# Kernel tuning notes

Hardware: AMD Instinct MI355X
Metric: run time of the kernel (lower is better)

## Reference

```python
import jax, jax.numpy as jnp
import numpy as np

N = 2_097_152  # total atoms
G = 32_768     # number of graphs (~64 atoms each)
EPS = 1e-4     # sign-detection threshold from the original code


def setup_inputs() -> dict:
    key = jax.random.key(0)
    k1, k2 = jax.random.split(key)
    pos = jax.random.normal(k1, (N, 3), dtype=jnp.float32) * 3.0
    batch = jnp.sort(jax.random.randint(k2, (N,), 0, G))
    return {"pos": pos, "batch": batch, "num_graphs": G}


def reference(pos, batch, num_graphs):
    n = pos.shape[0]
    dtype = pos.dtype

    # per-graph centroid (scatter_mean)
    counts = jax.ops.segment_sum(jnp.ones((n,), dtype), batch, num_segments=num_graphs)
    center = jax.ops.segment_sum(pos, batch, num_segments=num_graphs) / jnp.maximum(counts, 1.0)[:, None]
    pc = pos - center[batch]                      # [N,3] centered positions

    # per-atom inertia contribution: r^2 * I - p p^T, then scatter_add per graph
    r_sq = jnp.sum(pc * pc, axis=-1)              # [N]
    outer = jnp.einsum('ni,nj->nij', pc, pc)      # [N,3,3]
    I_atom = r_sq[:, None, None] * jnp.eye(3, dtype=dtype) - outer
    I_mol = jax.ops.segment_sum(I_atom, batch, num_segments=num_graphs)  # [G,3,3]

    L, Q = jnp.linalg.eigh(I_mol)                 # Q: [G,3,3], columns = principal axes

    # projections of centered positions onto the (pre-flip) eigenbasis.
    # NOTE: in the torch loop, p_proj is computed once before any sign flips, and
    # flipping column 0 does not affect p_proj[:,1], so axes 0 and 1 are independent.
    proj = jnp.einsum('ni,nij->nj', pc, Q[batch])  # [N,3]

    idx = jnp.arange(n)

    def axis_sign(a):
        # parallel "first atom (in original order) with |proj| > EPS" per graph
        qual = jnp.abs(proj[:, a]) > EPS
        key_idx = jnp.where(qual, idx, n)
        first = jax.ops.segment_min(key_idx, batch, num_segments=num_graphs)  # [G]
        found = first < n
        val = proj[jnp.minimum(first, n - 1), a]
        return jnp.where(found & (val < 0), -1.0, 1.0).astype(dtype)

    s0 = axis_sign(0)
    s1 = axis_sign(1)
    q0 = Q[:, :, 0] * s0[:, None]
    q1 = Q[:, :, 1] * s1[:, None]
    q2 = jnp.cross(q0, q1)  # enforce right-handed frame
    return jnp.stack([q0, q1, q2], axis=-1)       # [G,3,3]
```

## Files before the change

kernel.cpp:

```cpp
#include <hip/hip_runtime.h>
#include <math.h>

#define CANON_EPS 1e-4f

__global__ __launch_bounds__(256) void build_starts_kernel(
    const int* __restrict__ batch, int* __restrict__ wsi, int n, int G) {
  int t = (int)(blockIdx.x * (unsigned)blockDim.x + threadIdx.x);
  int base = t * 4;
  if (base >= n) return;

  int b0, b1, b2, b3;
  if (base + 4 <= n) {
    int4 b4 = *reinterpret_cast<const int4*>(batch + base);
    b0 = b4.x; b1 = b4.y; b2 = b4.z; b3 = b4.w;
  } else {
    b0 = batch[base];
    b1 = (base + 1 < n) ? batch[base + 1] : b0;
    b2 = (base + 2 < n) ? batch[base + 2] : b1;
    b3 = (base + 3 < n) ? batch[base + 3] : b2;
  }
  int bp = (base > 0) ? batch[base - 1] : -1;

  int B[4] = {b0, b1, b2, b3};
#pragma unroll
  for (int j = 0; j < 4; ++j) {
    int i = base + j;
    if (i >= n) break;
    int prev = (j == 0) ? bp : B[j - 1];
    int b = B[j];
    for (int g = prev + 1; g <= b; ++g) wsi[g] = i;
    if (i == n - 1) {
      for (int g = b + 1; g <= G; ++g) wsi[g] = n;
    }
  }
}

__global__ __launch_bounds__(256) void moments_kernel(
    const float* __restrict__ pos, const int* __restrict__ wsi,
    float* __restrict__ wsf, int G) {
  int tid = (int)(blockIdx.x * (unsigned)blockDim.x + threadIdx.x);
  int gid = tid >> 4;
  int sub = tid & 15;
  if (gid >= G) return;

  int s = wsi[gid];
  int e = wsi[gid + 1];
  int cnt = e - s;

  float sx = 0.f, sy = 0.f, sz = 0.f;
  float sxx = 0.f, syy = 0.f, szz = 0.f, sxy = 0.f, sxz = 0.f, syz = 0.f;

#pragma unroll
  for (int k = 0; k < 5; ++k) {
    int i = s + sub + 16 * k;
    bool in = i < e;
    int ii = in ? i : 0;
    float m = in ? 1.0f : 0.0f;
    float x = pos[3 * ii + 0] * m;
    float y = pos[3 * ii + 1] * m;
    float z = pos[3 * ii + 2] * m;
    sx += x; sy += y; sz += z;
    sxx = fmaf(x, x, sxx); syy = fmaf(y, y, syy); szz = fmaf(z, z, szz);
    sxy = fmaf(x, y, sxy); sxz = fmaf(x, z, sxz); syz = fmaf(y, z, syz);
  }
  for (int i = s + 80 + sub; i < e; i += 16) {
    float x = pos[3 * i + 0];
    float y = pos[3 * i + 1];
    float z = pos[3 * i + 2];
    sx += x; sy += y; sz += z;
    sxx = fmaf(x, x, sxx); syy = fmaf(y, y, szz * 0.f + syy); szz = fmaf(z, z, szz);
    sxy = fmaf(x, y, sxy); sxz = fmaf(x, z, sxz); syz = fmaf(y, z, syz);
  }

#define RED16(v)                                                             \
  v += __shfl_xor(v, 1); v += __shfl_xor(v, 2);                              \
  v += __shfl_xor(v, 4); v += __shfl_xor(v, 8);
  RED16(sx) RED16(sy) RED16(sz)
  RED16(sxx) RED16(syy) RED16(szz)
  RED16(sxy) RED16(sxz) RED16(syz)
#undef RED16

  float fn = (float)(cnt > 0 ? cnt : 1);
  float inv = 1.0f / fn;
  float mx = sx * inv, my = sy * inv, mz = sz * inv;
  float Sxx = fmaf(-fn * mx, mx, sxx);
  float Syy = fmaf(-fn * my, my, syy);
  float Szz = fmaf(-fn * mz, mz, szz);
  float Sxy = fmaf(-fn * mx, my, sxy);
  float Sxz = fmaf(-fn * mx, mz, sxz);
  float Syz = fmaf(-fn * my, mz, syz);

  float v = mx;
  v = (sub == 1) ? my : v;
  v = (sub == 2) ? mz : v;
  v = (sub == 3) ? (Syy + Szz) : v;
  v = (sub == 4) ? (Sxx + Szz) : v;
  v = (sub == 5) ? (Sxx + Syy) : v;
  v = (sub == 6) ? (-Sxy) : v;
  v = (sub == 7) ? (-Sxz) : v;
  v = (sub == 8) ? (-Syz) : v;
  if (sub < 9) wsf[(size_t)gid * 9 + sub] = v;
}

__device__ __forceinline__ void jacobi3_f32(float a00, float a11, float a22,
                                            float a01, float a02, float a12,
                                            float Q[3][3]) {
  float A00 = a00, A11 = a11, A22 = a22;
  float A01 = a01, A02 = a02, A12 = a12;
  float Q00 = 1.f, Q01 = 0.f, Q02 = 0.f;
  float Q10 = 0.f, Q11 = 1.f, Q12 = 0.f;
  float Q20 = 0.f, Q21 = 0.f, Q22 = 1.f;

#define ROT(App, Aqq, Apq, Akp, Akq, Qrp0, Qrq0, Qrp1, Qrq1, Qrp2, Qrq2)     \
  {                                                                          \
    float apq = Apq;                                                         \
    float theta = (Aqq - App) / (2.0f * apq);                                \
    float t = copysignf(1.0f, theta) /                                       \
              (fabsf(theta) + sqrtf(1.0f + theta * theta));                  \
    t = (apq == 0.0f) ? 0.0f : t;                    \
    float c = 1.0f / sqrtf(1.0f + t * t);                                    \
    float s = t * c;                                                         \
    App = App - t * apq;                                                     \
    Aqq = Aqq + t * apq;                                                     \
    Apq = 0.0f;                                                              \
    float akp = Akp, akq = Akq;                                              \
    Akp = c * akp - s * akq;                                                 \
    Akq = s * akp + c * akq;                                                 \
    float r0p = Qrp0, r0q = Qrq0;                                            \
    Qrp0 = c * r0p - s * r0q;                                                \
    Qrq0 = s * r0p + c * r0q;                                                \
    float r1p = Qrp1, r1q = Qrq1;                                            \
    Qrp1 = c * r1p - s * r1q;                                                \
    Qrq1 = s * r1p + c * r1q;                                                \
    float r2p = Qrp2, r2q = Qrq2;                                            \
    Qrp2 = c * r2p - s * r2q;                                                \
    Qrq2 = s * r2p + c * r2q;                                                \
  }

#pragma unroll
  for (int sweep = 0; sweep < 4; ++sweep) {
    ROT(A00, A11, A01, A02, A12, Q00, Q01, Q10, Q11, Q20, Q21);
    ROT(A00, A22, A02, A01, A12, Q00, Q02, Q10, Q12, Q20, Q22);
    ROT(A11, A22, A12, A01, A02, Q01, Q02, Q11, Q12, Q21, Q22);
  }
#undef ROT

  float w0 = A00, w1 = A11, w2 = A22;
#define CSWAP(wa, wb, qa0, qb0, qa1, qb1, qa2, qb2)                          \
  {                                                                          \
    bool sw = (wb) < (wa);                                                   \
    float tw = wa; wa = sw ? wb : wa; wb = sw ? tw : wb;                     \
    float t0 = qa0; qa0 = sw ? qb0 : qa0; qb0 = sw ? t0 : qb0;               \
    float t1 = qa1; qa1 = sw ? qb1 : qa1; qb1 = sw ? t1 : qb1;               \
    float t2 = qa2; qa2 = sw ? qb2 : qa2; qb2 = sw ? t2 : qb2;               \
  }
  CSWAP(w0, w1, Q00, Q01, Q10, Q11, Q20, Q21);
  CSWAP(w1, w2, Q01, Q02, Q11, Q12, Q21, Q22);
  CSWAP(w0, w1, Q00, Q01, Q10, Q11, Q20, Q21);
#undef CSWAP

  Q[0][0] = Q00; Q[0][1] = Q01; Q[0][2] = Q02;
  Q[1][0] = Q10; Q[1][1] = Q11; Q[1][2] = Q12;
  Q[2][0] = Q20; Q[2][1] = Q21; Q[2][2] = Q22;
}

__global__ __launch_bounds__(64) void eigen_kernel(
    const float* __restrict__ pos, const int* __restrict__ wsi,
    const float* __restrict__ wsf, float* __restrict__ out, int G) {
  int g = (int)(blockIdx.x * (unsigned)blockDim.x + threadIdx.x);
  if (g >= G) return;

  int s = wsi[g];
  int e = wsi[g + 1];

  const float* m = wsf + (size_t)g * 9;
  float cx  = m[0];
  float cy  = m[1];
  float cz  = m[2];
  float ixx = m[3];
  float iyy = m[4];
  float izz = m[5];
  float ixy = m[6];
  float ixz = m[7];
  float iyz = m[8];

  float px0, py0, pz0, px1, py1, pz1, px2, py2, pz2, px3, py3, pz3;
  {
    int i0 = (s + 0 < e) ? s + 0 : 0;
    int i1 = (s + 1 < e) ? s + 1 : 0;
    int i2 = (s + 2 < e) ? s + 2 : 0;
    int i3 = (s + 3 < e) ? s + 3 : 0;
    px0 = pos[3 * i0 + 0]; py0 = pos[3 * i0 + 1]; pz0 = pos[3 * i0 + 2];
    px1 = pos[3 * i1 + 0]; py1 = pos[3 * i1 + 1]; pz1 = pos[3 * i1 + 2];
    px2 = pos[3 * i2 + 0]; py2 = pos[3 * i2 + 1]; pz2 = pos[3 * i2 + 2];
    px3 = pos[3 * i3 + 0]; py3 = pos[3 * i3 + 1]; pz3 = pos[3 * i3 + 2];
  }

  float Q[3][3];
  jacobi3_f32(ixx, iyy, izz, ixy, ixz, iyz, Q);

  float q00 = Q[0][0], q10 = Q[1][0], q20 = Q[2][0];
  float q01 = Q[0][1], q11 = Q[1][1], q21 = Q[2][1];

  bool found0 = false, found1 = false;
  float v0 = 0.f, v1 = 0.f;
#define CHECK(PX, PY, PZ, J)                                                 \
  if (s + (J) < e) {                                                         \
    float x = (PX) - cx, y = (PY) - cy, z = (PZ) - cz;                       \
    float p0 = x * q00 + y * q10 + z * q20;                                  \
    float p1 = x * q01 + y * q11 + z * q21;                                  \
    if (!found0 && fabsf(p0) > CANON_EPS) { v0 = p0; found0 = true; }        \
    if (!found1 && fabsf(p1) > CANON_EPS) { v1 = p1; found1 = true; }        \
  }
  CHECK(px0, py0, pz0, 0)
  CHECK(px1, py1, pz1, 1)
  CHECK(px2, py2, pz2, 2)
  CHECK(px3, py3, pz3, 3)
#undef CHECK
  for (int i = s + 4; i < e && !(found0 && found1); ++i) {
    float x = pos[3 * i + 0] - cx;
    float y = pos[3 * i + 1] - cy;
    float z = pos[3 * i + 2] - cz;
    float p0 = x * q00 + y * q10 + z * q20;
    float p1 = x * q01 + y * q11 + z * q21;
    if (!found0 && fabsf(p0) > CANON_EPS) { v0 = p0; found0 = true; }
    if (!found1 && fabsf(p1) > CANON_EPS) { v1 = p1; found1 = true; }
  }
  float s0 = (found0 && v0 < 0.f) ? -1.f : 1.f;
  float s1 = (found1 && v1 < 0.f) ? -1.f : 1.f;

  float q0x = q00 * s0, q0y = q10 * s0, q0z = q20 * s0;
  float q1x = q01 * s1, q1y = q11 * s1, q1z = q21 * s1;
  float q2x = q0y * q1z - q0z * q1y;
  float q2y = q0z * q1x - q0x * q1z;
  float q2z = q0x * q1y - q0y * q1x;
  float* o = out + (size_t)g * 9;
  o[0] = q0x; o[1] = q1x; o[2] = q2x;
  o[3] = q0y; o[4] = q1y; o[5] = q2y;
  o[6] = q0z; o[7] = q1z; o[8] = q2z;
}

extern "C" void kernel_launch(void* const* d_in, const int* in_sizes, int n_in,
                              void* d_out, int out_size, void* d_ws, size_t ws_size,
                              hipStream_t stream) {
  const float* pos = (const float*)d_in[0];
  const int* batch = (const int*)d_in[1];
  float* out = (float*)d_out;

  int n = in_sizes[0] / 3;
  int G = out_size / 9;

  int* wsi = (int*)d_ws;
  float* wsf = (float*)((char*)d_ws + (((size_t)(G + 1) * 4 + 255) & ~255ull));

  int t1 = (n + 3) / 4;
  build_starts_kernel<<<(t1 + 255) / 256, 256, 0, stream>>>(batch, wsi, n, G);

  moments_kernel<<<(G * 16 + 255) / 256, 256, 0, stream>>>(pos, wsi, wsf, G);

  eigen_kernel<<<(G + 63) / 64, 64, 0, stream>>>(pos, wsi, wsf, out, G);
}
```

Baseline: 21.42 us.

## Fuse moments and eigen/sign kernels into one per-graph block kernel

Merges the moment-accumulation kernel and the eigen/sign-detection kernel into a single kernel that handles 16 graphs per 256-thread block. Each thread loads two contiguous 4-atom chunks as float4-sized structs. The per-graph moments and the first four atoms are staged in shared memory, so the 9-float workspace round trip and one kernel launch go away. The trade-off is that the Jacobi solve and sign scan now run on only 16 lanes per block, which leaves most of each block idle in that phase. Index clamping near the end of the array could also feed the wrong first atoms to a tiny final graph.

```diff
diff --git a/kernel.cpp b/kernel.cpp
--- a/kernel.cpp
+++ b/kernel.cpp
@@ -2,6 +2,8 @@
 #include <math.h>
 
 #define CANON_EPS 1e-4f
+
+struct f4u { float a, b, c, d; };
 
 __global__ __launch_bounds__(256) void build_starts_kernel(
     const int* __restrict__ batch, int* __restrict__ wsi, int n, int G) {
@@ -33,73 +35,6 @@
       for (int g = b + 1; g <= G; ++g) wsi[g] = n;
     }
   }
-}
-
-__global__ __launch_bounds__(256) void moments_kernel(
-    const float* __restrict__ pos, const int* __restrict__ wsi,
-    float* __restrict__ wsf, int G) {
-  int tid = (int)(blockIdx.x * (unsigned)blockDim.x + threadIdx.x);
-  int gid = tid >> 4;
-  int sub = tid & 15;
-  if (gid >= G) return;
-
-  int s = wsi[gid];
-  int e = wsi[gid + 1];
-  int cnt = e - s;
-
-  float sx = 0.f, sy = 0.f, sz = 0.f;
-  float sxx = 0.f, syy = 0.f, szz = 0.f, sxy = 0.f, sxz = 0.f, syz = 0.f;
-
-#pragma unroll
-  for (int k = 0; k < 5; ++k) {
-    int i = s + sub + 16 * k;
-    bool in = i < e;
-    int ii = in ? i : 0;
-    float m = in ? 1.0f : 0.0f;
-    float x = pos[3 * ii + 0] * m;
-    float y = pos[3 * ii + 1] * m;
-    float z = pos[3 * ii + 2] * m;
-    sx += x; sy += y; sz += z;
-    sxx = fmaf(x, x, sxx); syy = fmaf(y, y, syy); szz = fmaf(z, z, szz);
-    sxy = fmaf(x, y, sxy); sxz = fmaf(x, z, sxz); syz = fmaf(y, z, syz);
-  }
-  for (int i = s + 80 + sub; i < e; i += 16) {
-    float x = pos[3 * i + 0];
-    float y = pos[3 * i + 1];
-    float z = pos[3 * i + 2];
-    sx += x; sy += y; sz += z;
-    sxx = fmaf(x, x, sxx); syy = fmaf(y, y, szz * 0.f + syy); szz = fmaf(z, z, szz);
-    sxy = fmaf(x, y, sxy); sxz = fmaf(x, z, sxz); syz = fmaf(y, z, syz);
-  }
-
-#define RED16(v)                                                             \
-  v += __shfl_xor(v, 1); v += __shfl_xor(v, 2);                              \
-  v += __shfl_xor(v, 4); v += __shfl_xor(v, 8);
-  RED16(sx) RED16(sy) RED16(sz)
-  RED16(sxx) RED16(syy) RED16(szz)
-  RED16(sxy) RED16(sxz) RED16(syz)
-#undef RED16
-
-  float fn = (float)(cnt > 0 ? cnt : 1);
-  float inv = 1.0f / fn;
-  float mx = sx * inv, my = sy * inv, mz = sz * inv;
-  float Sxx = fmaf(-fn * mx, mx, sxx);
-  float Syy = fmaf(-fn * my, my, syy);
-  float Szz = fmaf(-fn * mz, mz, szz);
-  float Sxy = fmaf(-fn * mx, my, sxy);
-  float Sxz = fmaf(-fn * mx, mz, sxz);
-  float Syz = fmaf(-fn * my, mz, syz);
-
-  float v = mx;
-  v = (sub == 1) ? my : v;
-  v = (sub == 2) ? mz : v;
-  v = (sub == 3) ? (Syy + Szz) : v;
-  v = (sub == 4) ? (Sxx + Szz) : v;
-  v = (sub == 5) ? (Sxx + Syy) : v;
-  v = (sub == 6) ? (-Sxy) : v;
-  v = (sub == 7) ? (-Sxz) : v;
-  v = (sub == 8) ? (-Syz) : v;
-  if (sub < 9) wsf[(size_t)gid * 9 + sub] = v;
 }
 
 __device__ __forceinline__ void jacobi3_f32(float a00, float a11, float a22,
@@ -164,80 +99,146 @@
   Q[2][0] = Q20; Q[2][1] = Q21; Q[2][2] = Q22;
 }
 
-__global__ __launch_bounds__(64) void eigen_kernel(
+__global__ __launch_bounds__(256) void fused_kernel(
     const float* __restrict__ pos, const int* __restrict__ wsi,
-    const float* __restrict__ wsf, float* __restrict__ out, int G) {
-  int g = (int)(blockIdx.x * (unsigned)blockDim.x + threadIdx.x);
-  if (g >= G) return;
-
-  int s = wsi[g];
-  int e = wsi[g + 1];
-
-  const float* m = wsf + (size_t)g * 9;
-  float cx  = m[0];
-  float cy  = m[1];
-  float cz  = m[2];
-  float ixx = m[3];
-  float iyy = m[4];
-  float izz = m[5];
-  float ixy = m[6];
-  float ixz = m[7];
-  float iyz = m[8];
-
-  float px0, py0, pz0, px1, py1, pz1, px2, py2, pz2, px3, py3, pz3;
-  {
-    int i0 = (s + 0 < e) ? s + 0 : 0;
-    int i1 = (s + 1 < e) ? s + 1 : 0;
-    int i2 = (s + 2 < e) ? s + 2 : 0;
-    int i3 = (s + 3 < e) ? s + 3 : 0;
-    px0 = pos[3 * i0 + 0]; py0 = pos[3 * i0 + 1]; pz0 = pos[3 * i0 + 2];
-    px1 = pos[3 * i1 + 0]; py1 = pos[3 * i1 + 1]; pz1 = pos[3 * i1 + 2];
-    px2 = pos[3 * i2 + 0]; py2 = pos[3 * i2 + 1]; pz2 = pos[3 * i2 + 2];
-    px3 = pos[3 * i3 + 0]; py3 = pos[3 * i3 + 1]; pz3 = pos[3 * i3 + 2];
-  }
-
-  float Q[3][3];
-  jacobi3_f32(ixx, iyy, izz, ixy, ixz, iyz, Q);
-
-  float q00 = Q[0][0], q10 = Q[1][0], q20 = Q[2][0];
-  float q01 = Q[0][1], q11 = Q[1][1], q21 = Q[2][1];
-
-  bool found0 = false, found1 = false;
-  float v0 = 0.f, v1 = 0.f;
-#define CHECK(PX, PY, PZ, J)                                                 \
-  if (s + (J) < e) {                                                         \
-    float x = (PX) - cx, y = (PY) - cy, z = (PZ) - cz;                       \
+    float* __restrict__ out, int n, int G) {
+  __shared__ float lmom[16][9];
+  __shared__ float latm[16][12];
+  __shared__ int lsc[16][2];
+
+  int tid = (int)threadIdx.x;
+  int lg = tid >> 4;
+  int sub = tid & 15;
+  int gid = (int)blockIdx.x * 16 + lg;
+
+  int s = 0, e = 0;
+  if (gid < G) {
+    s = wsi[gid];
+    e = wsi[gid + 1];
+  }
+  int cnt = e - s;
+
+  int a0 = s + sub * 4;
+  int a1 = a0 + 64;
+  int c0 = min(a0, n - 4); c0 = c0 < 0 ? 0 : c0;
+  int c1 = min(a1, n - 4); c1 = c1 < 0 ? 0 : c1;
+  const f4u* p0 = reinterpret_cast<const f4u*>(pos + (size_t)3 * c0);
+  const f4u* p1 = reinterpret_cast<const f4u*>(pos + (size_t)3 * c1);
+  f4u v0 = p0[0], v1 = p0[1], v2 = p0[2];
+  f4u u0 = p1[0], u1 = p1[1], u2 = p1[2];
+
+  float sx = 0.f, sy = 0.f, sz = 0.f;
+  float sxx = 0.f, syy = 0.f, szz = 0.f, sxy = 0.f, sxz = 0.f, syz = 0.f;
+  int rem = cnt - sub * 4;
+
+#define ACC3(X, Y, Z, V)                                                     \
+  {                                                                          \
+    float m = (V) ? 1.0f : 0.0f;                                             \
+    float x = (X) * m, y = (Y) * m, z = (Z) * m;                             \
+    sx += x; sy += y; sz += z;                                               \
+    sxx = fmaf(x, x, sxx); syy = fmaf(y, y, syy); szz = fmaf(z, z, szz);     \
+    sxy = fmaf(x, y, sxy); sxz = fmaf(x, z, sxz); syz = fmaf(y, z, syz);     \
+  }
+  ACC3(v0.a, v0.b, v0.c, 0 < rem)
+  ACC3(v0.d, v1.a, v1.b, 1 < rem)
+  ACC3(v1.c, v1.d, v2.a, 2 < rem)
+  ACC3(v2.b, v2.c, v2.d, 3 < rem)
+  ACC3(u0.a, u0.b, u0.c, 64 < rem)
+  ACC3(u0.d, u1.a, u1.b, 65 < rem)
+  ACC3(u1.c, u1.d, u2.a, 66 < rem)
+  ACC3(u2.b, u2.c, u2.d, 67 < rem)
+  for (int i = s + 128 + sub; i < e; i += 16) {
+    float x = pos[3 * i + 0], y = pos[3 * i + 1], z = pos[3 * i + 2];
+    sx += x; sy += y; sz += z;
+    sxx = fmaf(x, x, sxx); syy = fmaf(y, y, syy); szz = fmaf(z, z, szz);
+    sxy = fmaf(x, y, sxy); sxz = fmaf(x, z, sxz); syz = fmaf(y, z, syz);
+  }
+#undef ACC3
+
+#define RED16(v)                                                             \
+  v += __shfl_xor(v, 1); v += __shfl_xor(v, 2);                              \
+  v += __shfl_xor(v, 4); v += __shfl_xor(v, 8);
+  RED16(sx) RED16(sy) RED16(sz)
+  RED16(sxx) RED16(syy) RED16(szz)
+  RED16(sxy) RED16(sxz) RED16(syz)
+#undef RED16
+
+  if (sub == 0 && gid < G) {
+    float fn = (float)(cnt > 0 ? cnt : 1);
+    float inv = 1.0f / fn;
+    float mx = sx * inv, my = sy * inv, mz = sz * inv;
+    float Sxx = fmaf(-fn * mx, mx, sxx);
+    float Syy = fmaf(-fn * my, my, syy);
+    float Szz = fmaf(-fn * mz, mz, szz);
+    float Sxy = fmaf(-fn * mx, my, sxy);
+    float Sxz = fmaf(-fn * mx, mz, sxz);
+    float Syz = fmaf(-fn * my, mz, syz);
+    lmom[lg][0] = mx; lmom[lg][1] = my; lmom[lg][2] = mz;
+    lmom[lg][3] = Syy + Szz;
+    lmom[lg][4] = Sxx + Szz;
+    lmom[lg][5] = Sxx + Syy;
+    lmom[lg][6] = -Sxy;
+    lmom[lg][7] = -Sxz;
+    lmom[lg][8] = -Syz;
+    latm[lg][0] = v0.a; latm[lg][1] = v0.b; latm[lg][2]  = v0.c;
+    latm[lg][3] = v0.d; latm[lg][4] = v1.a; latm[lg][5]  = v1.b;
+    latm[lg][6] = v1.c; latm[lg][7] = v1.d; latm[lg][8]  = v2.a;
+    latm[lg][9] = v2.b; latm[lg][10] = v2.c; latm[lg][11] = v2.d;
+    lsc[lg][0] = s; lsc[lg][1] = cnt;
+  }
+  __syncthreads();
+
+  if (tid < 16) {
+    int g = (int)blockIdx.x * 16 + tid;
+    if (g < G) {
+      float cx = lmom[tid][0], cy = lmom[tid][1], cz = lmom[tid][2];
+      float Q[3][3];
+      jacobi3_f32(lmom[tid][3], lmom[tid][4], lmom[tid][5], lmom[tid][6],
+                  lmom[tid][7], lmom[tid][8], Q);
+
+      float q00 = Q[0][0], q10 = Q[1][0], q20 = Q[2][0];
+      float q01 = Q[0][1], q11 = Q[1][1], q21 = Q[2][1];
+
+      int s2 = lsc[tid][0];
+      int cnt2 = lsc[tid][1];
+
+      bool found0 = false, found1 = false;
+      float v0s = 0.f, v1s = 0.f;
+#define CHECK(J)                                                             \
+  if ((J) < cnt2) {                                                          \
+    float x = latm[tid][3 * (J) + 0] - cx;                                   \
+    float y = latm[tid][3 * (J) + 1] - cy;                                   \
+    float z = latm[tid][3 * (J) + 2] - cz;                                   \
     float p0 = x * q00 + y * q10 + z * q20;                                  \
     float p1 = x * q01 + y * q11 + z * q21;                                  \
-    if (!found0 && fabsf(p0) > CANON_EPS) { v0 = p0; found0 = true; }        \
-    if (!found1 && fabsf(p1) > CANON_EPS) { v1 = p1; found1 = true; }        \
-  }
-  CHECK(px0, py0, pz0, 0)
-  CHECK(px1, py1, pz1, 1)
-  CHECK(px2, py2, pz2, 2)
-  CHECK(px3, py3, pz3, 3)
+    if (!found0 && fabsf(p0) > CANON_EPS) { v0s = p0; found0 = true; }       \
+    if (!found1 && fabsf(p1) > CANON_EPS) { v1s = p1; found1 = true; }       \
+  }
+      CHECK(0) CHECK(1) CHECK(2) CHECK(3)
 #undef CHECK
-  for (int i = s + 4; i < e && !(found0 && found1); ++i) {
-    float x = pos[3 * i + 0] - cx;
-    float y = pos[3 * i + 1] - cy;
-    float z = pos[3 * i + 2] - cz;
-    float p0 = x * q00 + y * q10 + z * q20;
-    float p1 = x * q01 + y * q11 + z * q21;
-    if (!found0 && fabsf(p0) > CANON_EPS) { v0 = p0; found0 = true; }
-    if (!found1 && fabsf(p1) > CANON_EPS) { v1 = p1; found1 = true; }
-  }
-  float s0 = (found0 && v0 < 0.f) ? -1.f : 1.f;
-  float s1 = (found1 && v1 < 0.f) ? -1.f : 1.f;
-
-  float q0x = q00 * s0, q0y = q10 * s0, q0z = q20 * s0;
-  float q1x = q01 * s1, q1y = q11 * s1, q1z = q21 * s1;
-  float q2x = q0y * q1z - q0z * q1y;
-  float q2y = q0z * q1x - q0x * q1z;
-  float q2z = q0x * q1y - q0y * q1x;
-  float* o = out + (size_t)g * 9;
-  o[0] = q0x; o[1] = q1x; o[2] = q2x;
-  o[3] = q0y; o[4] = q1y; o[5] = q2y;
-  o[6] = q0z; o[7] = q1z; o[8] = q2z;
+      for (int i = s2 + 4; i < s2 + cnt2 && !(found0 && found1); ++i) {
+        float x = pos[3 * i + 0] - cx;
+        float y = pos[3 * i + 1] - cy;
+        float z = pos[3 * i + 2] - cz;
+        float p0 = x * q00 + y * q10 + z * q20;
+        float p1 = x * q01 + y * q11 + z * q21;
+        if (!found0 && fabsf(p0) > CANON_EPS) { v0s = p0; found0 = true; }
+        if (!found1 && fabsf(p1) > CANON_EPS) { v1s = p1; found1 = true; }
+      }
+      float s0 = (found0 && v0s < 0.f) ? -1.f : 1.f;
+      float s1 = (found1 && v1s < 0.f) ? -1.f : 1.f;
+
+      float q0x = q00 * s0, q0y = q10 * s0, q0z = q20 * s0;
+      float q1x = q01 * s1, q1y = q11 * s1, q1z = q21 * s1;
+      float q2x = q0y * q1z - q0z * q1y;
+      float q2y = q0z * q1x - q0x * q1z;
+      float q2z = q0x * q1y - q0y * q1x;
+      float* o = out + (size_t)g * 9;
+      o[0] = q0x; o[1] = q1x; o[2] = q2x;
+      o[3] = q0y; o[4] = q1y; o[5] = q2y;
+      o[6] = q0z; o[7] = q1z; o[8] = q2z;
+    }
+  }
 }
 
 extern "C" void kernel_launch(void* const* d_in, const int* in_sizes, int n_in,
@@ -251,12 +252,9 @@
   int G = out_size / 9;
 
   int* wsi = (int*)d_ws;
-  float* wsf = (float*)((char*)d_ws + (((size_t)(G + 1) * 4 + 255) & ~255ull));
 
   int t1 = (n + 3) / 4;
   build_starts_kernel<<<(t1 + 255) / 256, 256, 0, stream>>>(batch, wsi, n, G);
 
-  moments_kernel<<<(G * 16 + 255) / 256, 256, 0, stream>>>(pos, wsi, wsf, G);
-
-  eigen_kernel<<<(G + 63) / 64, 64, 0, stream>>>(pos, wsi, wsf, out, G);
-}
+  fused_kernel<<<(G + 15) / 16, 256, 0, stream>>>(pos, wsi, out, n, G);
+}
```

After: 23.22 us. 8.4% more time.
